# Kernel optimization log

Hardware: AMD Instinct MI355X
Metric: run time of the kernel (lower is better)

## Reference

```python
import jax, jax.numpy as jnp
import numpy as np

V = 50000      # tokenizer vocab size
E = 128        # embedding_dim
H = 160        # encoder_hidden_dim (bidirectional -> 2H)
D = 196        # decoder_hidden_dim
A = 224        # attention_dim
BN = 56        # bottle_neck_dim
PAD, START, END, UNK = 0, 1, 2, 3
COV_FACTOR = 0.75


def _lstm_step(x, h, c, Wi, Wh, bi, bh):
    # torch gate order: i, f, g, o
    g = x @ Wi.T + h @ Wh.T + bi + bh
    i, f, gg, o = jnp.split(g, 4, axis=-1)
    c = jax.nn.sigmoid(f) * c + jax.nn.sigmoid(i) * jnp.tanh(gg)
    h = jax.nn.sigmoid(o) * jnp.tanh(c)
    return h, c


def _run_lstm(x_tbe, Wi, Wh, bi, bh):
    B = x_tbe.shape[1]
    Hh = Wh.shape[1]
    def step(carry, xt):
        h, c = carry
        h, c = _lstm_step(xt, h, c, Wi, Wh, bi, bh)
        return (h, c), h
    init = (jnp.zeros((B, Hh), x_tbe.dtype), jnp.zeros((B, Hh), x_tbe.dtype))
    (hT, cT), hs = jax.lax.scan(step, init, x_tbe)
    return hs, hT, cT


def setup_inputs() -> dict:
    key = jax.random.key(0)
    ks = iter(jax.random.split(key, 48))
    def rn(shape, s=0.05):
        return jax.random.normal(next(ks), shape, jnp.float32) * s
    B, Tin, Ttgt = 32, 256, 100
    inp = {
        'batch_input_ids': jax.random.randint(next(ks), (B, Tin), 0, V + 50, dtype=jnp.int32),
        'batch_target_ids': jax.random.randint(next(ks), (B, Ttgt), 0, V + 50, dtype=jnp.int32),
        'max_num_oovs': 50,
        'emb': rn((V, E), 0.1),
        # bidirectional encoder LSTM
        'Wi_f': rn((4 * H, E)), 'Wh_f': rn((4 * H, H)),
        'bi_f': jnp.zeros(4 * H), 'bh_f': jnp.zeros(4 * H),
        'Wi_b': rn((4 * H, E)), 'Wh_b': rn((4 * H, H)),
        'bi_b': jnp.zeros(4 * H), 'bh_b': jnp.zeros(4 * H),
        # enc->dec bridges
        'Weh': rn((D, 2 * H)), 'beh': jnp.zeros(D),
        'Wec': rn((D, 2 * H)), 'bec': jnp.zeros(D),
        # decoder LSTMCell
        'Wi_d': rn((4 * D, E)), 'Wh_d': rn((4 * D, D)),
        'bi_d': jnp.zeros(4 * D), 'bh_d': jnp.zeros(4 * D),
        # attention
        'Wea': rn((A, 2 * H)), 'bea': jnp.zeros(A),
        'Wda': rn((A, D)),
        'Wca': rn((A, 1)),
        'v_attn': rn((1, A)),
        # vocab projection (bottleneck)
        'W1': rn((BN, D + 2 * H)), 'b1': jnp.zeros(BN),
        'W2': rn((V - END, BN)), 'b2': jnp.zeros(V - END),
        # p_gen switch
        'Wcs': rn((1, 2 * H)), 'bcs': jnp.zeros(1),
        'Wds': rn((1, D)),
        'Wes': rn((1, E)),
    }
    return inp


def reference(batch_input_ids, batch_target_ids, max_num_oovs, emb,
              Wi_f, Wh_f, bi_f, bh_f, Wi_b, Wh_b, bi_b, bh_b,
              Weh, beh, Wec, bec, Wi_d, Wh_d, bi_d, bh_d,
              Wea, bea, Wda, Wca, v_attn, W1, b1, W2, b2,
              Wcs, bcs, Wds, Wes):
    B, Tin = batch_input_ids.shape
    # map OOV input ids to <unk> for embedding lookup
    in_mapped = jnp.where(batch_input_ids >= V, UNK, batch_input_ids)
    x_tbe = emb[in_mapped].transpose(1, 0, 2)          # [Tin,B,E]
    hs_f, hTf, cTf = _run_lstm(x_tbe, Wi_f, Wh_f, bi_f, bh_f)
    hs_b, hTb, cTb = _run_lstm(x_tbe[::-1], Wi_b, Wh_b, bi_b, bh_b)
    enc = jnp.concatenate([hs_f, hs_b[::-1]], -1).transpose(1, 0, 2)  # [B,Tin,2H]
    h = jnp.concatenate([hTf, hTb], -1) @ Weh.T + beh   # [B,D]
    c = jnp.concatenate([cTf, cTb], -1) @ Wec.T + bec   # [B,D]
    enc_attn = enc @ Wea.T + bea                        # [B,Tin,A] (loop-invariant)
    pad_mask = batch_input_ids == PAD
    wca = Wca[:, 0]                                     # [A]
    cov0 = jnp.zeros((B, Tin))
    cur0 = jnp.full((B,), START, jnp.int32)

    def step(carry, nt):
        h, c, cov, cur, nll, cl = carry
        e = emb[cur]                                     # [B,E]
        h, c = _lstm_step(e, h, c, Wi_d, Wh_d, bi_d, bh_d)
        s = jnp.tanh(enc_attn + (h @ Wda.T)[:, None, :] + cov[:, :, None] * wca)
        s = s @ v_attn[0]                                # [B,Tin]
        s = jnp.where(pad_mask, -jnp.inf, s)
        attn = jax.nn.softmax(s, axis=1)                 # [B,Tin]
        ctx = jnp.einsum('bt,bth->bh', attn, enc)        # [B,2H]
        hc = jnp.concatenate([h, ctx], -1)
        vocab = jax.nn.softmax(jnp.tanh(hc @ W1.T + b1) @ W2.T + b2, axis=1)  # [B,V-END]
        p_gen = jax.nn.sigmoid(ctx @ Wcs[0] + bcs[0] + h @ Wds[0] + e @ Wes[0])  # [B]
        # F.pad(vocab, (END, max_num_oovs)).gather(1, nt): left-pad END zeros,
        # right-pad OOV zeros -> gen prob is vocab[nt-END] if END<=nt<V else 0
        idx = jnp.clip(nt - END, 0, vocab.shape[1] - 1)
        gen_p = jnp.take_along_axis(vocab, idx[:, None], axis=1)[:, 0]
        gen_p = jnp.where((nt >= END) & (nt < V), gen_p, 0.0)
        copy_p = jnp.sum(attn * (batch_input_ids == nt[:, None]), axis=1)
        p = p_gen * gen_p + (1.0 - p_gen) * copy_p
        nll = nll - jnp.log(p + 1e-9)
        cl = cl + jnp.minimum(attn, cov).sum(axis=1)
        cov = cov + attn
        cur = jnp.where(nt >= V, UNK, nt)
        return (h, c, cov, cur, nll, cl), None

    (h, c, cov, cur, nll, cl), _ = jax.lax.scan(
        step, (h, c, cov0, cur0, jnp.zeros(B), jnp.zeros(B)), batch_target_ids.T)
    nll_loss = nll.sum()
    cov_loss = cl.sum()
    return nll_loss, cov_loss, nll_loss + COV_FACTOR * cov_loss
```

## Files before the change

kernel.cpp:

```cpp
#include <hip/hip_runtime.h>

#define MSCOPE __HIP_MEMORY_SCOPE_AGENT

typedef __attribute__((ext_vector_type(8))) short bf16x8;
typedef __attribute__((ext_vector_type(4))) float f32x4;


constexpr size_t oXf   = 0;
constexpr size_t oXb   = oXf   + (size_t)8192*640;
constexpr size_t oXd   = oXb   + (size_t)8192*640;
constexpr size_t oHencB= oXd   + (size_t)3200*784;
constexpr size_t oEncA = oHencB+ (size_t)64*256*160;
constexpr size_t oEs   = oEncA + (size_t)8192*224;
constexpr size_t oCT   = oEs   + 3200;
constexpr size_t oH0   = oCT   + 10240;
constexpr size_t oC0   = oH0   + 6272;
constexpr size_t oHWdsAll = oC0 + 6272;
constexpr size_t oCtxWAll = oHWdsAll + 3200;
constexpr size_t oCopyAll = oCtxWAll + 3200;
constexpr size_t oZidxAll = oCopyAll + 3200;
constexpr size_t oClAll   = oZidxAll + 3200;
constexpr size_t oNllWg   = oClAll + 32;
constexpr size_t oW1cT    = oNllWg + 224;
constexpr size_t oAFl     = oW1cT + 17920;
constexpr size_t oAFa     = oAFl + 93184;
constexpr size_t oHdF     = oAFa + 32256;
constexpr size_t oFEnd    = oHdF + 358400;
constexpr size_t oUAll    = 0;
constexpr size_t oUPreAll = oUAll  + (size_t)100*1792;
constexpr size_t oHwdaAll = oUPreAll + (size_t)100*1792;
constexpr size_t oPartAll = oHwdaAll + (size_t)100*7168;
#define FENC(d,t,p)  ((((d)*256 + (t))*20 + (p))*16)
#define FLSTM(s,p)   (163840 + ((s)*8 + (p))*16)
#define FAUX(s,p)    (176640 + ((s)*8 + (p))*16)
#define FP2(s,m,b)   (189440 + (((s)*4 + (m))*32 + (b))*16)
#define CP3          394240
#define CFIN         394256
constexpr int fEnd = 394272;
constexpr unsigned ENC_FULL  = 0xFFFFFu;

__device__ __forceinline__ float fast_tanh(float x){
  float e = __expf(-2.f*fabsf(x));
  float r = (1.f - e) * __builtin_amdgcn_rcpf(1.f + e);
  return copysignf(r, x);
}
__device__ __forceinline__ float sigm(float x){
  return __builtin_amdgcn_rcpf(1.f + __expf(-x));
}
__device__ __forceinline__ unsigned bfr(float f){
  unsigned u = __float_as_uint(f);
  return (u + 0x7FFFu + ((u>>16)&1u)) >> 16;
}
__device__ __forceinline__ float aload(const float* p){
  return __hip_atomic_load(const_cast<float*>(p), __ATOMIC_RELAXED, MSCOPE);
}
__device__ __forceinline__ float2 aload2(const float* p){
  unsigned long long u = __hip_atomic_load(
      reinterpret_cast<unsigned long long*>(const_cast<float*>(p)),
      __ATOMIC_RELAXED, MSCOPE);
  float2 r; __builtin_memcpy(&r, &u, 8); return r;
}
__device__ __forceinline__ void astore(float* p, float v){
  __hip_atomic_store(p, v, __ATOMIC_RELAXED, MSCOPE);
}
__device__ __forceinline__ void astoreu(unsigned* p, unsigned v){
  __hip_atomic_store(p, v, __ATOMIC_RELAXED, MSCOPE);
}
__device__ __forceinline__ void astore2(float* p, float a, float b){
  float2 t; t.x = a; t.y = b;
  unsigned long long u; __builtin_memcpy(&u, &t, 8);
  __hip_atomic_store(reinterpret_cast<unsigned long long*>(p), u,
                     __ATOMIC_RELAXED, MSCOPE);
}
__device__ __forceinline__ unsigned uload(unsigned* p){
  return __hip_atomic_load(p, __ATOMIC_RELAXED, MSCOPE);
}
__device__ __forceinline__ void set_line(unsigned* line){
  __hip_atomic_store(line, 1u, __ATOMIC_RELAXED, MSCOPE);
}
template<int SLP>
__device__ __forceinline__ void wait_lines(unsigned* base, int n, int tid){
  if (tid < 64){
    for(;;){
      bool miss = (tid < n) && (uload(base + tid*16) == 0u);
      if (__ballot(miss) == 0ULL) break;
      __builtin_amdgcn_s_sleep(SLP);
    }
  }
  __syncthreads();
}
__device__ __forceinline__ void add1(unsigned* word){
  (void)__hip_atomic_fetch_add(word, 1u, __ATOMIC_RELAXED, MSCOPE);
}
__device__ __forceinline__ float block_sum(float v, float* red){
  #pragma unroll
  for (int o=32;o;o>>=1) v += __shfl_down(v,o);
  if ((threadIdx.x&63)==0) red[threadIdx.x>>6] = v;
  __syncthreads();
  v = red[0]+red[1]+red[2]+red[3];
  __syncthreads();
  return v;
}

__global__ void prep_kernel(const int* __restrict__ in_ids, const int* __restrict__ tgt,
                            int* __restrict__ in_mapped, int* __restrict__ cur_ids,
                            unsigned* __restrict__ flags, float* __restrict__ hdF){
  const int g0 = blockIdx.x*256 + threadIdx.x, stride = gridDim.x*256;
  for (int i = g0; i < 8192; i += stride){
    int t = i >> 5, b = i & 31;
    int id = in_ids[b*256 + t];
    in_mapped[i] = (id >= 50000) ? 3 : id;
  }
  for (int i = g0; i < 3200; i += stride){
    int k = i >> 5, b = i & 31;
    int id = (k == 0) ? 1 : tgt[b*100 + (k-1)];
    cur_ids[i] = (id >= 50000) ? 3 : id;
  }
  for (int i = g0; i < fEnd; i += stride) flags[i] = 0u;
  for (int i = g0; i < 358400; i += stride) hdF[i] = 0.f;
}

__global__ void w1c_transpose(const float* __restrict__ W1, float* __restrict__ W1cT){
  int i = blockIdx.x*256 + threadIdx.x;
  if (i < 17920){ int q = i / 56, g = i - q*56; W1cT[q*56+g] = W1[(size_t)g*516 + 196 + q]; }
}

__global__ void pack_af(const float* __restrict__ Whd, float* __restrict__ AFl,
                        const float* __restrict__ Wda, const float* __restrict__ W1,
                        const float* __restrict__ Wds, float* __restrict__ AFa){
  int dw = blockIdx.x*256 + threadIdx.x;
  if (dw < 93184){
    int frag = dw>>2, d = dw&3;
    int T = frag/448, r2 = frag - T*448;
    int k7 = r2>>6, l = r2&63;
    int jb = T>>2, gate = T&3;
    int j = jb*16 + (l&15);
    int k0 = k7*32 + ((l>>4)<<3) + 2*d;
    unsigned lo=0, hi=0;
    if (j < 196){
      if (k0   < 196) lo = bfr(Whd[(size_t)(gate*196+j)*196 + k0]);
      if (k0+1 < 196) hi = bfr(Whd[(size_t)(gate*196+j)*196 + k0+1]);
    }
    ((unsigned*)AFl)[dw] = lo | (hi<<16);
  }
  if (dw < 32256){
    int frag = dw>>2, d = dw&3;
    int T = frag/448, r2 = frag - T*448;
    int k7 = r2>>6, l = r2&63;
    int ar = T*16 + (l&15);
    int k0 = k7*32 + ((l>>4)<<3) + 2*d;
    unsigned lo=0, hi=0;
    #pragma unroll
    for (int h = 0; h < 2; ++h){
      int k = k0 + h;
      float v = 0.f;
      if (k < 196){
        if (ar < 224) v = Wda[(size_t)ar*196 + k];
        else { int g = ar - 224;
          if (g < 56) v = W1[(size_t)g*516 + k];
          else if (g == 56) v = Wds[k];
        }
      }
      if (h == 0) lo = bfr(v); else hi = bfr(v);
    }
    ((unsigned*)AFa)[dw] = lo | (hi<<16);
  }
}

struct RGArgs{ const int* gid; const float* emb; const float* W;
               const float* bias1; const float* bias2; float* out; int N; };
__global__ void __launch_bounds__(256) rowgemm(RGArgs a){
  __shared__ float rl[8*128];
  const int tid = threadIdx.x;
  const int N = a.N;
  const size_t r0 = (size_t)blockIdx.x*8;
  const size_t t = r0 >> 5; const int b0 = (int)(r0 & 31);
  for (int i = tid; i < 8*128; i += 256){
    int r = i >> 7, k = i & 127;
    rl[i] = a.emb[(size_t)a.gid[r0+r]*128 + k];
  }
  __syncthreads();
  for (int g = tid; g < N; g += 256){
    const float* wr = a.W + (size_t)g*128;
    float acc[8];
    #pragma unroll
    for (int r=0;r<8;r++) acc[r]=0.f;
    for (int k=0;k<128;k+=4){
      float4 wv = *(const float4*)(wr+k);
      #pragma unroll
      for (int r=0;r<8;r++){
        float4 xv = *(const float4*)(rl + r*128 + k);
        acc[r] += wv.x*xv.x + wv.y*xv.y + wv.z*xv.z + wv.w*xv.w;
      }
    }
    float bias = a.bias1[g] + a.bias2[g];
    float* op = a.out + ((size_t)t*N + g)*32 + b0;
    *(float4*)(op)   = make_float4(acc[0]+bias,acc[1]+bias,acc[2]+bias,acc[3]+bias);
    *(float4*)(op+4) = make_float4(acc[4]+bias,acc[5]+bias,acc[6]+bias,acc[7]+bias);
  }
}

__global__ void es_kernel(const int* __restrict__ gid, const float* __restrict__ emb,
                          const float* __restrict__ Wes, float* __restrict__ es){
  int r = blockIdx.x, l = threadIdx.x;
  const float* e = emb + (size_t)gid[r]*128;
  float acc = e[l]*Wes[l] + e[l+64]*Wes[l+64];
  #pragma unroll
  for (int o=32;o;o>>=1) acc += __shfl_down(acc,o);
  if (l==0) es[r] = acc;
}

struct EncArgs{ const float* Xf; const float* Xb; const float* Whf; const float* Whb;
                float* hencB; float* cT; unsigned* flg; };
__global__ void __launch_bounds__(256) enc_scan(EncArgs a){
  extern __shared__ float sm[];
  float* Wl = sm;
  float* hl = sm + 5120;
  const int wg = blockIdx.x;
  const int dir = wg/20, jwg = wg%20;
  const int tid = threadIdx.x;
  const int b = tid & 31, jl = tid >> 5;
  const int j = jwg*8 + jl;
  const float* Wh = dir ? a.Whb : a.Whf;
  const float* X  = dir ? a.Xb  : a.Xf;
  float* HB = a.hencB + (size_t)dir*32*256*160;
  unsigned* flg = a.flg;
  for (int i = tid; i < 32*160; i += 256){
    int row = i/160, k = i - row*160;
    int gate = row >> 3, jj = row & 7;
    Wl[i] = Wh[((size_t)(gate*160 + jwg*8 + jj))*160 + k];
  }
  for (int i = tid; i < 32*164; i += 256) hl[i] = 0.f;
  float c = 0.f;
  const float4* w0 = (const float4*)(Wl + (0*8+jl)*160);
  const float4* w1 = (const float4*)(Wl + (1*8+jl)*160);
  const float4* w2 = (const float4*)(Wl + (2*8+jl)*160);
  const float4* w3 = (const float4*)(Wl + (3*8+jl)*160);
  __syncthreads();
  for (int t = 0; t < 256; ++t){
    const int trow = dir ? 255 - t : t;
    const float* xr = X + ((size_t)trow*640 + j)*32 + b;
    float g0 = xr[0], g1 = xr[5120], g2 = xr[10240], g3 = xr[15360];
    if (t > 0){
      wait_lines<2>(flg + FENC(dir, t-1, 0), 20, tid);
      const int tprev = dir ? (256 - t) : (t-1);
      for (int i2 = tid; i2 < 2560; i2 += 256){
        int bb = i2/80, kk = (i2 - bb*80)*2;
        float2 v = aload2(HB + ((size_t)bb*256 + tprev)*160 + kk);
        *(float2*)(hl + bb*164 + kk) = v;
      }
    }
    __syncthreads();
    const float4* hr = (const float4*)(hl + b*164);
    #pragma unroll 4
    for (int q = 0; q < 40; ++q){
      float4 hv = hr[q];
      float4 a0 = w0[q], a1 = w1[q], a2 = w2[q], a3 = w3[q];
      g0 += hv.x*a0.x + hv.y*a0.y + hv.z*a0.z + hv.w*a0.w;
      g1 += hv.x*a1.x + hv.y*a1.y + hv.z*a1.z + hv.w*a1.w;
      g2 += hv.x*a2.x + hv.y*a2.y + hv.z*a2.z + hv.w*a2.w;
      g3 += hv.x*a3.x + hv.y*a3.y + hv.z*a3.z + hv.w*a3.w;
    }
    float ig = sigm(g0), fg = sigm(g1), gc = fast_tanh(g2), og = sigm(g3);
    c = fg*c + ig*gc;
    float h = og * fast_tanh(c);
    astore(&HB[((size_t)b*256 + trow)*160 + j], h);
    __syncthreads();
    if (tid == 0) set_line(flg + FENC(dir, t, jwg));
  }
  a.cT[dir*5120 + b*160 + j] = c;
}

__global__ void mid_kernel(const float* __restrict__ hencB, const float* __restrict__ cT,
                           const float* __restrict__ Weh, const float* __restrict__ beh,
                           const float* __restrict__ Wec, const float* __restrict__ bec,
                           float* __restrict__ h0, float* __restrict__ c0){
  __shared__ float hc[320], cc[320];
  int b = blockIdx.x, tid = threadIdx.x;
  if (tid < 160){
    hc[tid]     = hencB[((size_t)b*256 + 255)*160 + tid];
    hc[160+tid] = hencB[((size_t)(32+b)*256 + 0)*160 + tid];
    cc[tid]     = cT[b*160 + tid];
    cc[160+tid] = cT[5120 + b*160 + tid];
  }
  __syncthreads();
  for (int g = tid; g < 196; g += 256){
    const float* w1 = Weh + (size_t)g*320;
    const float* w2 = Wec + (size_t)g*320;
    float a1 = beh[g], a2 = bec[g];
    for (int k = 0; k < 320; ++k){ a1 += hc[k]*w1[k]; a2 += cc[k]*w2[k]; }
    h0[b*196 + g] = a1;
    c0[b*196 + g] = a2;
  }
}

__global__ void __launch_bounds__(256) encA_gemm(const float* __restrict__ hencB,
                 const float* __restrict__ Wea, const float* __restrict__ bea,
                 float* __restrict__ encA){
  __shared__ float rl[8*320];
  const int tid = threadIdx.x;
  const size_t r0 = (size_t)blockIdx.x*8;
  for (int i = tid; i < 8*320; i += 256){
    int r = i/320, k = i - r*320;
    size_t row = r0 + r; int b = (int)(row >> 8), t = (int)(row & 255);
    rl[i] = (k < 160) ? hencB[((size_t)b*256 + t)*160 + k]
                      : hencB[((size_t)(32+b)*256 + t)*160 + (k-160)];
  }
  __syncthreads();
  for (int g = tid; g < 224; g += 256){
    const float* wr = Wea + (size_t)g*320;
    float acc[8];
    #pragma unroll
    for (int r=0;r<8;r++) acc[r]=0.f;
    for (int k=0;k<320;k+=4){
      float4 wv = *(const float4*)(wr+k);
      #pragma unroll
      for (int r=0;r<8;r++){
        float4 xv = *(const float4*)(rl + r*320 + k);
        acc[r] += wv.x*xv.x + wv.y*xv.y + wv.z*xv.z + wv.w*xv.w;
      }
    }
    float bias = bea[g];
    #pragma unroll
    for (int r=0;r<8;r++) encA[(r0+r)*224 + g] = acc[r] + bias;
  }
}

struct DecArgs{
  const float* Xd; const float* hencB; const float* encA;
  const float* h0; const float* c0; const float* AFl; const float* AFa;
  float* hdF;
  const float* Wca; const float* vat; const float* W1cT; const float* b1;
  const float* W2; const float* b2;
  const float* Wcs; const float* bcs; const float* es;
  const int* in_ids; const int* tgt;
  float* uAll; float* uPreAll; float* hwdaAll;
  float* hWdsAll; float* ctxWAll; float* copyAll;
  float* zidxAll; float* partAll; float* clAll; float* nllWg; float* out;
  unsigned* flg;
};

__global__ void __launch_bounds__(256) dec_scan(DecArgs A){
  extern __shared__ float sm[];
  const int wg = blockIdx.x, tid = threadIdx.x;
  unsigned* flg = A.flg;

  if (wg < 8){
    const int q = wg;
    const int nUq  = (q < 5) ? 2 : 1;
    const int jb0q = q;
    const int jb1q = (q < 5) ? q + 8 : 0;
    const int auxB = (q < 5) ? q : (q == 5 ? 5 : (q == 6 ? 9 : 13));
    const int auxC = (q < 5) ? 1 : (q == 7 ? 5 : 4);
    unsigned* ldsu = (unsigned*)sm;
    bf16x8*   ldsf = (bf16x8*)sm;
    const int AB = nUq*1792;
    const int l = tid & 63, wv = tid >> 6;
    const int lq = l >> 4, lc = l & 15;
    const int u = wv >> 1, nt = wv & 1;
    const bool act = u < nUq;
    const int jb = (u == 0) ? jb0q : jb1q;
    {
      const unsigned* aflu = (const unsigned*)A.AFl;
      const unsigned* afau = (const unsigned*)A.AFa;
      const int totDw = (AB + auxC*448)*4;
      for (int i = tid; i < totDw; i += 256){
        int slot = i>>2, d = i&3;
        unsigned v;
        if (slot < AB){
          int uu = slot/1792, r = slot - uu*1792;
          int fi = r>>6, ll = r&63;
          int jbu = (uu == 0) ? jb0q : jb1q;
          int T = jbu*4 + fi/7, k7 = fi%7;
          v = aflu[(((size_t)T*7 + k7)*64 + ll)*4 + d];
        } else {
          int r = slot - AB;
          int a = r/448, r2 = r - a*448;
          int k7 = r2>>6, ll = r2&63;
          v = afau[((((size_t)(auxB + a))*7 + k7)*64 + ll)*4 + d];
        }
        ldsu[i] = v;
      }
    }
    float cst[4];
    if (act){
      int b = nt*16 + lc;
      #pragma unroll
      for (int i = 0; i < 4; ++i){
        int j = jb*16 + lq*4 + i;
        cst[i] = (j < 196) ? A.c0[b*196 + j] : 0.f;
      }
    }
    bf16x8 Bfr[7][2];
    #pragma unroll
    for (int k7 = 0; k7 < 7; ++k7)
      #pragma unroll
      for (int ntt = 0; ntt < 2; ++ntt){
        short tmp[8];
        #pragma unroll
        for (int e = 0; e < 8; ++e){
          int k = k7*32 + lq*8 + e;
          int b = ntt*16 + lc;
          float hv = (k < 196) ? A.h0[b*196 + k] : 0.f;
          tmp[e] = (short)bfr(hv);
        }
        __builtin_memcpy(&Bfr[k7][ntt], tmp, 16);
      }
    __syncthreads();
    unsigned* hdF = (unsigned*)A.hdF;
    for (int s = 0; s < 100; ++s){
      const float* Xs = A.Xd + (size_t)s*25088;
      if (act){
        float xg4[4][4];
        #pragma unroll
        for (int g = 0; g < 4; ++g)
          #pragma unroll
          for (int i = 0; i < 4; ++i){
            int j = jb*16 + lq*4 + i;
            int b = nt*16 + lc;
            xg4[g][i] = (j < 196) ? Xs[((size_t)(g*196 + j))*32 + b] : 0.f;
          }
        f32x4 acc[4];
        #pragma unroll
        for (int g = 0; g < 4; ++g){
          f32x4 a0 = {0.f,0.f,0.f,0.f};
          #pragma unroll
          for (int k7 = 0; k7 < 7; ++k7){
            bf16x8 af = ldsf[(u*28 + g*7 + k7)*64 + l];
            a0 = __builtin_amdgcn_mfma_f32_16x16x32_bf16(af, Bfr[k7][nt], a0, 0,0,0);
          }
          acc[g] = a0;
        }
        float hv4[4];
        #pragma unroll
        for (int i = 0; i < 4; ++i){
          float I = acc[0][i]+xg4[0][i], F = acc[1][i]+xg4[1][i];
          float G = acc[2][i]+xg4[2][i], O = acc[3][i]+xg4[3][i];
          float cc = sigm(F)*cst[i] + sigm(I)*fast_tanh(G);
          cst[i] = cc;
          hv4[i] = sigm(O)*fast_tanh(cc);
        }
        #pragma unroll
        for (int p = 0; p < 2; ++p){
          int jp = jb*16 + lq*4 + 2*p;
          if (jp < 196){
            int k7 = jp>>5, tl = lc | (((jp>>3)&3)<<4), d = (jp&7)>>1;
            unsigned w = bfr(hv4[2*p]) | (bfr(hv4[2*p+1])<<16);
            astoreu(&hdF[(size_t)s*3584 + ((k7*2+nt)*64 + tl)*4 + d], w);
          }
        }
      }
      __syncthreads();
      if (tid == 0) set_line(flg + FLSTM(s, q));
      wait_lines<1>(flg + FLSTM(s, 0), 8, tid);
      {
        const float* hp = (const float*)(hdF + (size_t)s*3584);
        #pragma unroll
        for (int k7 = 0; k7 < 7; ++k7)
          #pragma unroll
          for (int ntt = 0; ntt < 2; ++ntt){
            float2 v0 = aload2(hp + (((k7*2+ntt)*64 + l)*4));
            float2 v1 = aload2(hp + (((k7*2+ntt)*64 + l)*4 + 2));
            unsigned dwv[4];
            __builtin_memcpy(dwv, &v0, 8); __builtin_memcpy(dwv+2, &v1, 8);
            __builtin_memcpy(&Bfr[k7][ntt], dwv, 16);
          }
      }
      for (int a = wv; a < auxC; a += 4){
        int T = auxB + a;
        #pragma unroll
        for (int ntt = 0; ntt < 2; ++ntt){
          f32x4 acc = {0.f,0.f,0.f,0.f};
          #pragma unroll
          for (int k7 = 0; k7 < 7; ++k7){
            bf16x8 af = ldsf[AB + (a*7 + k7)*64 + l];
            acc = __builtin_amdgcn_mfma_f32_16x16x32_bf16(af, Bfr[k7][ntt], acc, 0,0,0);
          }
          int b = ntt*16 + lc;
          #pragma unroll
          for (int p = 0; p < 2; ++p){
            int ar = T*16 + lq*4 + 2*p;
            float v0 = acc[2*p], v1 = acc[2*p+1];
            if (ar < 224){
              astore2(&A.hwdaAll[(size_t)s*7168 + b*224 + ar], v0, v1);
            } else {
              int g = ar - 224;
              if (g < 56) astore2(&A.uPreAll[(size_t)s*1792 + b*56 + g], v0, v1);
              else if (g == 56) astore(&A.hWdsAll[s*32 + b], v0);
            }
          }
        }
      }
      __syncthreads();
      if (tid == 0) set_line(flg + FAUX(s, q));
    }
    return;
  }

  if (wg < 40){
    const int b = wg - 8;
    float* hwdaL = sm;
    float* attnL = sm + 224;
    float* pctx  = sm + 480;
    float* ctxL  = sm + 1440;
    float* red   = sm + 1760;
    float* pu    = sm + 1764;
    float* wcaL  = sm + 1988;
    float* vL    = sm + 2212;
    float* WcsL  = sm + 2436;
    float* b1L   = sm + 2756;
    if (tid < 224){ wcaL[tid] = A.Wca[tid]; vL[tid] = A.vat[tid]; }
    for (int i = tid; i < 320; i += 256) WcsL[i] = A.Wcs[i];
    if (tid < 56) b1L[tid] = A.b1[tid];
    const int inid = A.in_ids[b*256 + tid];
    const float4* erow = (const float4*)(A.encA + (size_t)(b*256 + tid)*224);
    float cov = 0.f, clr = 0.f;
    __syncthreads();
    for (int s = 0; s < 100; ++s){
      wait_lines<2>(flg + FAUX(s, 0), 8, tid);
      if (tid < 224) hwdaL[tid] = aload(&A.hwdaAll[(size_t)s*7168 + b*224 + tid]);
      __syncthreads();
      float exv = 0.f;
      if (inid != 0){
        float acc = 0.f;
        #pragma unroll 8
        for (int q = 0; q < 56; ++q){
          float4 ev = erow[q]; int a0 = 4*q;
          acc += fast_tanh(ev.x + hwdaL[a0]   + cov*wcaL[a0]  )*vL[a0];
          acc += fast_tanh(ev.y + hwdaL[a0+1] + cov*wcaL[a0+1])*vL[a0+1];
          acc += fast_tanh(ev.z + hwdaL[a0+2] + cov*wcaL[a0+2])*vL[a0+2];
          acc += fast_tanh(ev.w + hwdaL[a0+3] + cov*wcaL[a0+3])*vL[a0+3];
        }
        exv = __expf(acc);
      }
      float S = block_sum(exv, red);
      float attn = exv * __builtin_amdgcn_rcpf(S);
      attnL[tid] = attn;
      const int ntb = A.tgt[b*100 + s];
      float cpS = block_sum((inid == ntb) ? attn : 0.f, red);
      float mnS = block_sum(fminf(attn, cov), red);
      if (tid == 0){
        astore(&A.copyAll[s*32 + b], cpS);
        clr += mnS;
        if (s == 99) astore(&A.clAll[b], clr);
      }
      cov += attn;
      if (tid < 240){
        int seg = tid/80, h4i = tid - seg*80;
        int t0 = seg*86, t1 = (t0+86 < 256) ? t0+86 : 256;
        const float* base = (h4i < 40)
          ? (A.hencB + ((size_t)b*256)*160 + (size_t)h4i*4)
          : (A.hencB + ((size_t)(32+b)*256)*160 + (size_t)(h4i-40)*4);
        float4 accv = {0.f,0.f,0.f,0.f};
        #pragma unroll 4
        for (int t2 = t0; t2 < t1; ++t2){
          float av = attnL[t2];
          float4 ev = *(const float4*)(base + (size_t)t2*160);
          accv.x += av*ev.x; accv.y += av*ev.y; accv.z += av*ev.z; accv.w += av*ev.w;
        }
        *(float4*)(pctx + (seg*80+h4i)*4) = accv;
      }
      __syncthreads();
      if (tid < 80){
        float4 p0 = *(float4*)(pctx + tid*4);
        float4 p1 = *(float4*)(pctx + (80+tid)*4);
        float4 p2v = *(float4*)(pctx + (160+tid)*4);
        float4 cvv;
        cvv.x = p0.x+p1.x+p2v.x; cvv.y = p0.y+p1.y+p2v.y;
        cvv.z = p0.z+p1.z+p2v.z; cvv.w = p0.w+p1.w+p2v.w;
        *(float4*)(ctxL + tid*4) = cvv;
      }
      __syncthreads();
      if (tid < 224){
        int g = tid % 56, seg = tid / 56;
        float acc = 0.f;
        const float* wp = A.W1cT + (size_t)seg*80*56 + g;
        #pragma unroll 4
        for (int q = 0; q < 80; ++q) acc += ctxL[seg*80 + q] * wp[q*56];
        pu[seg*56 + g] = acc;
      } else {
        int l = tid - 224; float acc = 0.f;
        for (int q = l; q < 320; q += 32) acc += ctxL[q]*WcsL[q];
        #pragma unroll
        for (int o=16;o;o>>=1) acc += __shfl_down(acc,o,32);
        if (l==0) astore(&A.ctxWAll[s*32 + b], acc);
      }
      __syncthreads();
      if (tid < 56){
        float upre = aload(&A.uPreAll[(size_t)s*1792 + b*56 + tid]);
        float uu = fast_tanh(upre + b1L[tid] + pu[tid] + pu[56+tid] + pu[112+tid] + pu[168+tid]);
        astore(&A.uAll[(size_t)s*1792 + b*56 + tid], uu);
      }
      __syncthreads();
      if (tid == 0){
        set_line(flg + FP2(s,0,b));
        set_line(flg + FP2(s,1,b));
        set_line(flg + FP2(s,2,b));
        set_line(flg + FP2(s,3,b));
      }
    }
    return;
  }

  {
    const int wgv = wg - 40;
    const int vs = (int)(((long long)wgv*49998)/216);
    const int ve = (int)(((long long)(wgv+1)*49998)/216);
    const int v = vs + tid;
    const bool valid = v < ve;
    const int vc = valid ? v : 0;
    float4 w2r[14];
    {
      const float4* wr = (const float4*)(A.W2 + (size_t)vc*56);
      #pragma unroll
      for (int q=0;q<14;++q) w2r[q] = wr[q];
    }
    const float b2v = A.b2[vc];
    float* ulL  = sm;
    float* redW = sm + 1792;
    int*   idxL = (int*)(sm + 1920);
    float* red  = sm + 1952;
    const int lane = tid & 63, wv2 = tid >> 6;
    for (int s = 0; s < 100; ++s){
      int nt3 = (tid < 32) ? A.tgt[tid*100 + s] : 0;
      wait_lines<8>(flg + FP2(s, wgv & 3, 0), 32, tid);
      for (int i2 = tid; i2 < 896; i2 += 256){
        float2 u2 = aload2(&A.uAll[(size_t)s*1792 + i2*2]);
        *(float2*)(ulL + i2*2) = u2;
      }
      if (tid < 32){
        int ix = nt3 - 2; ix = ix<0?0:(ix>49997?49997:ix);
        idxL[tid] = ix;
      }
      __syncthreads();
      #pragma unroll 4
      for (int bb=0; bb<32; ++bb){
        const float4* uv = (const float4*)(ulL + bb*56);
        float z = b2v;
        #pragma unroll
        for (int q=0;q<14;++q){
          float4 u4 = uv[q];
          z += w2r[q].x*u4.x + w2r[q].y*u4.y + w2r[q].z*u4.z + w2r[q].w*u4.w;
        }
        if (valid && v == idxL[bb]) astore(&A.zidxAll[s*32+bb], z);
        float sv2 = valid ? __expf(z) : 0.f;
        #pragma unroll
        for (int o=32;o;o>>=1) sv2 += __shfl_down(sv2,o);
        if (lane == 0) redW[wv2*32+bb] = sv2;
      }
      __syncthreads();
      if (tid < 32){
        float tot = redW[tid]+redW[32+tid]+redW[64+tid]+redW[96+tid];
        astore(&A.partAll[(size_t)(s*32+tid)*216 + wgv], tot);
      }
      __syncthreads();
    }
    __syncthreads();
    if (tid == 0) add1(flg + CP3);
    if (tid == 0){
      while (uload(flg + CP3) != 216u) __builtin_amdgcn_s_sleep(32);
    }
    __syncthreads();
    float nll1 = 0.f;
    for (int p = wgv; p < 3200; p += 216){
      float pv = (tid < 216) ? aload(&A.partAll[(size_t)p*216 + tid]) : 0.f;
      float se = block_sum(pv, red);
      if (tid == 0){
        int s = p >> 5, b = p & 31;
        int nt2 = A.tgt[b*100 + s];
        float xg = aload(&A.ctxWAll[p]) + A.bcs[0] + aload(&A.hWdsAll[p]) + A.es[p];
        float pg = 1.f/(1.f + __expf(-xg));
        float genp = (nt2 >= 2 && nt2 < 50000) ? (__expf(aload(&A.zidxAll[p])) / se) : 0.f;
        float pr = pg*genp + (1.f-pg)*aload(&A.copyAll[p]);
        nll1 += -logf(pr + 1e-9f);
      }
    }
    if (tid == 0) astore(&A.nllWg[wgv], nll1);
    __syncthreads();
    if (tid == 0) add1(flg + CFIN);
    if (wg == 40){
      if (tid == 0){
        while (uload(flg + CFIN) != 216u) __builtin_amdgcn_s_sleep(32);
      }
      __syncthreads();
      float nv = (tid < 216) ? aload(&A.nllWg[tid]) : 0.f;
      float nll = block_sum(nv, red);
      float cv = (tid < 32) ? aload(&A.clAll[tid]) : 0.f;
      float cl = block_sum(cv, red);
      if (tid == 0){ A.out[0]=nll; A.out[1]=cl; A.out[2]=nll + 0.75f*cl; }
    }
  }
}

extern "C" void kernel_launch(void* const* d_in, const int* in_sizes, int n_in,
                              void* d_out, int out_size, void* d_ws, size_t ws_size,
                              hipStream_t stream){
  const int*   in_ids = (const int*)  d_in[0];
  const int*   tgt    = (const int*)  d_in[1];
  const float* emb    = (const float*)d_in[3];
  const float* Wi_f   = (const float*)d_in[4];
  const float* Wh_f   = (const float*)d_in[5];
  const float* bi_f   = (const float*)d_in[6];
  const float* bh_f   = (const float*)d_in[7];
  const float* Wi_b   = (const float*)d_in[8];
  const float* Wh_b   = (const float*)d_in[9];
  const float* bi_b   = (const float*)d_in[10];
  const float* bh_b   = (const float*)d_in[11];
  const float* Weh    = (const float*)d_in[12];
  const float* beh    = (const float*)d_in[13];
  const float* Wec    = (const float*)d_in[14];
  const float* bec    = (const float*)d_in[15];
  const float* Wi_d   = (const float*)d_in[16];
  const float* Wh_d   = (const float*)d_in[17];
  const float* bi_d   = (const float*)d_in[18];
  const float* bh_d   = (const float*)d_in[19];
  const float* Wea    = (const float*)d_in[20];
  const float* bea    = (const float*)d_in[21];
  const float* Wda    = (const float*)d_in[22];
  const float* Wca    = (const float*)d_in[23];
  const float* vat    = (const float*)d_in[24];
  const float* W1     = (const float*)d_in[25];
  const float* b1     = (const float*)d_in[26];
  const float* W2     = (const float*)d_in[27];
  const float* b2     = (const float*)d_in[28];
  const float* Wcs    = (const float*)d_in[29];
  const float* bcs    = (const float*)d_in[30];
  const float* Wds    = (const float*)d_in[31];
  const float* Wes    = (const float*)d_in[32];

  float* ws = (float*)d_ws;
  int* iBase = (int*)(ws + oFEnd);
  int* in_mapped = iBase;
  int* cur_ids   = iBase + 8192;
  unsigned* flags = (unsigned*)(iBase + 11392);

  prep_kernel<<<512, 256, 0, stream>>>(in_ids, tgt, in_mapped, cur_ids, flags,
                                       ws + oHdF);
  w1c_transpose<<<70, 256, 0, stream>>>(W1, ws + oW1cT);
  pack_af<<<364, 256, 0, stream>>>(Wh_d, ws + oAFl, Wda, W1, Wds, ws + oAFa);

  { RGArgs a{in_mapped, emb, Wi_f, bi_f, bh_f, ws + oXf, 640};
    rowgemm<<<1024, 256, 0, stream>>>(a); }
  { RGArgs a{in_mapped, emb, Wi_b, bi_b, bh_b, ws + oXb, 640};
    rowgemm<<<1024, 256, 0, stream>>>(a); }
  { RGArgs a{cur_ids, emb, Wi_d, bi_d, bh_d, ws + oXd, 784};
    rowgemm<<<400, 256, 0, stream>>>(a); }

  es_kernel<<<3200, 64, 0, stream>>>(cur_ids, emb, Wes, ws + oEs);

  { EncArgs ea{ws + oXf, ws + oXb, Wh_f, Wh_b, ws + oHencB, ws + oCT, flags};
    void* ka[] = {&ea};
    hipLaunchCooperativeKernel((void*)enc_scan, dim3(40), dim3(256), ka,
                               (unsigned)((5120 + 32*164)*4), stream); }

  mid_kernel<<<32, 256, 0, stream>>>(ws + oHencB, ws + oCT, Weh, beh, Wec, bec,
                                     ws + oH0, ws + oC0);

  encA_gemm<<<1024, 256, 0, stream>>>(ws + oHencB, Wea, bea, ws + oEncA);

  { DecArgs da{ws + oXd, ws + oHencB, ws + oEncA,
               ws + oH0, ws + oC0, ws + oAFl, ws + oAFa,
               ws + oHdF,
               Wca, vat, ws + oW1cT, b1, W2, b2, Wcs, bcs, ws + oEs,
               in_ids, tgt,
               ws + oUAll, ws + oUPreAll, ws + oHwdaAll,
               ws + oHWdsAll, ws + oCtxWAll, ws + oCopyAll,
               ws + oZidxAll, ws + oPartAll, ws + oClAll, ws + oNllWg, (float*)d_out,
               flags};
    dec_scan<<<dim3(256), dim3(256), 64512, stream>>>(da); }
}
```

Baseline: 4.650 ms.

## Fold independent prep work into encoder scan launch and move encA GEMM into decoder

The decoder-input GEMM, weight packing, W1 transpose and es dot products now run as extra blocks of the same launch as the 40-block encoder recurrence, so they fill otherwise idle CUs while the latency-bound scan runs. The separate encA GEMM kernel is removed. Its work is now done inside the decoder's vocab workgroups before their main loop, and a counter flag tells the attention workgroups when encA is complete. This removes several launches and hides their work behind the serial scan. In exchange, the encoder scan is no longer a cooperative launch, so it relies on its 40 spin-waiting blocks all being resident at once. The encA GEMM also becomes a less efficient one-row-at-a-time loop on the decoder's critical path.

```diff
diff --git a/kernel.cpp b/kernel.cpp
--- a/kernel.cpp
+++ b/kernel.cpp
@@ -36,7 +36,8 @@
 #define FP2(s,m,b)   (189440 + (((s)*4 + (m))*32 + (b))*16)
 #define CP3          394240
 #define CFIN         394256
-constexpr int fEnd = 394272;
+#define CENC         394272
+constexpr int fEnd = 394288;
 constexpr unsigned ENC_FULL  = 0xFFFFFu;
 
 __device__ __forceinline__ float fast_tanh(float x){
@@ -118,53 +119,6 @@
   }
   for (int i = g0; i < fEnd; i += stride) flags[i] = 0u;
   for (int i = g0; i < 358400; i += stride) hdF[i] = 0.f;
-}
-
-__global__ void w1c_transpose(const float* __restrict__ W1, float* __restrict__ W1cT){
-  int i = blockIdx.x*256 + threadIdx.x;
-  if (i < 17920){ int q = i / 56, g = i - q*56; W1cT[q*56+g] = W1[(size_t)g*516 + 196 + q]; }
-}
-
-__global__ void pack_af(const float* __restrict__ Whd, float* __restrict__ AFl,
-                        const float* __restrict__ Wda, const float* __restrict__ W1,
-                        const float* __restrict__ Wds, float* __restrict__ AFa){
-  int dw = blockIdx.x*256 + threadIdx.x;
-  if (dw < 93184){
-    int frag = dw>>2, d = dw&3;
-    int T = frag/448, r2 = frag - T*448;
-    int k7 = r2>>6, l = r2&63;
-    int jb = T>>2, gate = T&3;
-    int j = jb*16 + (l&15);
-    int k0 = k7*32 + ((l>>4)<<3) + 2*d;
-    unsigned lo=0, hi=0;
-    if (j < 196){
-      if (k0   < 196) lo = bfr(Whd[(size_t)(gate*196+j)*196 + k0]);
-      if (k0+1 < 196) hi = bfr(Whd[(size_t)(gate*196+j)*196 + k0+1]);
-    }
-    ((unsigned*)AFl)[dw] = lo | (hi<<16);
-  }
-  if (dw < 32256){
-    int frag = dw>>2, d = dw&3;
-    int T = frag/448, r2 = frag - T*448;
-    int k7 = r2>>6, l = r2&63;
-    int ar = T*16 + (l&15);
-    int k0 = k7*32 + ((l>>4)<<3) + 2*d;
-    unsigned lo=0, hi=0;
-    #pragma unroll
-    for (int h = 0; h < 2; ++h){
-      int k = k0 + h;
-      float v = 0.f;
-      if (k < 196){
-        if (ar < 224) v = Wda[(size_t)ar*196 + k];
-        else { int g = ar - 224;
-          if (g < 56) v = W1[(size_t)g*516 + k];
-          else if (g == 56) v = Wds[k];
-        }
-      }
-      if (h == 0) lo = bfr(v); else hi = bfr(v);
-    }
-    ((unsigned*)AFa)[dw] = lo | (hi<<16);
-  }
 }
 
 struct RGArgs{ const int* gid; const float* emb; const float* W;
@@ -200,75 +154,166 @@
   }
 }
 
-__global__ void es_kernel(const int* __restrict__ gid, const float* __restrict__ emb,
-                          const float* __restrict__ Wes, float* __restrict__ es){
-  int r = blockIdx.x, l = threadIdx.x;
-  const float* e = emb + (size_t)gid[r]*128;
-  float acc = e[l]*Wes[l] + e[l+64]*Wes[l+64];
-  #pragma unroll
-  for (int o=32;o;o>>=1) acc += __shfl_down(acc,o);
-  if (l==0) es[r] = acc;
-}
-
-struct EncArgs{ const float* Xf; const float* Xb; const float* Whf; const float* Whb;
-                float* hencB; float* cT; unsigned* flg; };
-__global__ void __launch_bounds__(256) enc_scan(EncArgs a){
+struct MegaArgs{
+  const float* Xf; const float* Xb; const float* Whf; const float* Whb;
+  float* hencB; float* cT; unsigned* flg;
+  const int* cur_ids; const float* emb;
+  const float* Wi_d; const float* bi_d; const float* bh_d; float* Xd;
+  const float* Whd; float* AFl;
+  const float* Wda; const float* W1; const float* Wds; float* AFa;
+  float* W1cT;
+  const float* Wes; float* es;
+};
+
+__global__ void __launch_bounds__(256) enc_mega(MegaArgs a){
   extern __shared__ float sm[];
-  float* Wl = sm;
-  float* hl = sm + 5120;
-  const int wg = blockIdx.x;
-  const int dir = wg/20, jwg = wg%20;
-  const int tid = threadIdx.x;
-  const int b = tid & 31, jl = tid >> 5;
-  const int j = jwg*8 + jl;
-  const float* Wh = dir ? a.Whb : a.Whf;
-  const float* X  = dir ? a.Xb  : a.Xf;
-  float* HB = a.hencB + (size_t)dir*32*256*160;
-  unsigned* flg = a.flg;
-  for (int i = tid; i < 32*160; i += 256){
-    int row = i/160, k = i - row*160;
-    int gate = row >> 3, jj = row & 7;
-    Wl[i] = Wh[((size_t)(gate*160 + jwg*8 + jj))*160 + k];
-  }
-  for (int i = tid; i < 32*164; i += 256) hl[i] = 0.f;
-  float c = 0.f;
-  const float4* w0 = (const float4*)(Wl + (0*8+jl)*160);
-  const float4* w1 = (const float4*)(Wl + (1*8+jl)*160);
-  const float4* w2 = (const float4*)(Wl + (2*8+jl)*160);
-  const float4* w3 = (const float4*)(Wl + (3*8+jl)*160);
-  __syncthreads();
-  for (int t = 0; t < 256; ++t){
-    const int trow = dir ? 255 - t : t;
-    const float* xr = X + ((size_t)trow*640 + j)*32 + b;
-    float g0 = xr[0], g1 = xr[5120], g2 = xr[10240], g3 = xr[15360];
-    if (t > 0){
-      wait_lines<2>(flg + FENC(dir, t-1, 0), 20, tid);
-      const int tprev = dir ? (256 - t) : (t-1);
-      for (int i2 = tid; i2 < 2560; i2 += 256){
-        int bb = i2/80, kk = (i2 - bb*80)*2;
-        float2 v = aload2(HB + ((size_t)bb*256 + tprev)*160 + kk);
-        *(float2*)(hl + bb*164 + kk) = v;
-      }
-    }
+  const int blk = blockIdx.x, tid = threadIdx.x;
+
+  if (blk < 40){
+    float* Wl = sm;
+    float* hl = sm + 5120;
+    const int dir = blk/20, jwg = blk%20;
+    const int b = tid & 31, jl = tid >> 5;
+    const int j = jwg*8 + jl;
+    const float* Wh = dir ? a.Whb : a.Whf;
+    const float* X  = dir ? a.Xb  : a.Xf;
+    float* HB = a.hencB + (size_t)dir*32*256*160;
+    unsigned* flg = a.flg;
+    for (int i = tid; i < 32*160; i += 256){
+      int row = i/160, k = i - row*160;
+      int gate = row >> 3, jj = row & 7;
+      Wl[i] = Wh[((size_t)(gate*160 + jwg*8 + jj))*160 + k];
+    }
+    for (int i = tid; i < 32*164; i += 256) hl[i] = 0.f;
+    float c = 0.f;
+    const float4* w0 = (const float4*)(Wl + (0*8+jl)*160);
+    const float4* w1 = (const float4*)(Wl + (1*8+jl)*160);
+    const float4* w2 = (const float4*)(Wl + (2*8+jl)*160);
+    const float4* w3 = (const float4*)(Wl + (3*8+jl)*160);
     __syncthreads();
-    const float4* hr = (const float4*)(hl + b*164);
-    #pragma unroll 4
-    for (int q = 0; q < 40; ++q){
-      float4 hv = hr[q];
-      float4 a0 = w0[q], a1 = w1[q], a2 = w2[q], a3 = w3[q];
-      g0 += hv.x*a0.x + hv.y*a0.y + hv.z*a0.z + hv.w*a0.w;
-      g1 += hv.x*a1.x + hv.y*a1.y + hv.z*a1.z + hv.w*a1.w;
-      g2 += hv.x*a2.x + hv.y*a2.y + hv.z*a2.z + hv.w*a2.w;
-      g3 += hv.x*a3.x + hv.y*a3.y + hv.z*a3.z + hv.w*a3.w;
-    }
-    float ig = sigm(g0), fg = sigm(g1), gc = fast_tanh(g2), og = sigm(g3);
-    c = fg*c + ig*gc;
-    float h = og * fast_tanh(c);
-    astore(&HB[((size_t)b*256 + trow)*160 + j], h);
+    for (int t = 0; t < 256; ++t){
+      const int trow = dir ? 255 - t : t;
+      const float* xr = X + ((size_t)trow*640 + j)*32 + b;
+      float g0 = xr[0], g1 = xr[5120], g2 = xr[10240], g3 = xr[15360];
+      if (t > 0){
+        wait_lines<2>(flg + FENC(dir, t-1, 0), 20, tid);
+        const int tprev = dir ? (256 - t) : (t-1);
+        for (int i2 = tid; i2 < 2560; i2 += 256){
+          int bb = i2/80, kk = (i2 - bb*80)*2;
+          float2 v = aload2(HB + ((size_t)bb*256 + tprev)*160 + kk);
+          *(float2*)(hl + bb*164 + kk) = v;
+        }
+      }
+      __syncthreads();
+      const float4* hr = (const float4*)(hl + b*164);
+      #pragma unroll 4
+      for (int q = 0; q < 40; ++q){
+        float4 hv = hr[q];
+        float4 a0 = w0[q], a1 = w1[q], a2 = w2[q], a3 = w3[q];
+        g0 += hv.x*a0.x + hv.y*a0.y + hv.z*a0.z + hv.w*a0.w;
+        g1 += hv.x*a1.x + hv.y*a1.y + hv.z*a1.z + hv.w*a1.w;
+        g2 += hv.x*a2.x + hv.y*a2.y + hv.z*a2.z + hv.w*a2.w;
+        g3 += hv.x*a3.x + hv.y*a3.y + hv.z*a3.z + hv.w*a3.w;
+      }
+      float ig = sigm(g0), fg = sigm(g1), gc = fast_tanh(g2), og = sigm(g3);
+      c = fg*c + ig*gc;
+      float h = og * fast_tanh(c);
+      astore(&HB[((size_t)b*256 + trow)*160 + j], h);
+      __syncthreads();
+      if (tid == 0) set_line(flg + FENC(dir, t, jwg));
+    }
+    a.cT[dir*5120 + b*160 + j] = c;
+    return;
+  }
+
+  if (blk < 440){
+    float* rl = sm;
+    const size_t r0 = (size_t)(blk - 40)*8;
+    const size_t t = r0 >> 5; const int b0 = (int)(r0 & 31);
+    for (int i = tid; i < 8*128; i += 256){
+      int r = i >> 7, k = i & 127;
+      rl[i] = a.emb[(size_t)a.cur_ids[r0+r]*128 + k];
+    }
     __syncthreads();
-    if (tid == 0) set_line(flg + FENC(dir, t, jwg));
-  }
-  a.cT[dir*5120 + b*160 + j] = c;
+    for (int g = tid; g < 784; g += 256){
+      const float* wr = a.Wi_d + (size_t)g*128;
+      float acc[8];
+      #pragma unroll
+      for (int r=0;r<8;r++) acc[r]=0.f;
+      for (int k=0;k<128;k+=4){
+        float4 wv = *(const float4*)(wr+k);
+        #pragma unroll
+        for (int r=0;r<8;r++){
+          float4 xv = *(const float4*)(rl + r*128 + k);
+          acc[r] += wv.x*xv.x + wv.y*xv.y + wv.z*xv.z + wv.w*xv.w;
+        }
+      }
+      float bias = a.bi_d[g] + a.bh_d[g];
+      float* op = a.Xd + ((size_t)t*784 + g)*32 + b0;
+      *(float4*)(op)   = make_float4(acc[0]+bias,acc[1]+bias,acc[2]+bias,acc[3]+bias);
+      *(float4*)(op+4) = make_float4(acc[4]+bias,acc[5]+bias,acc[6]+bias,acc[7]+bias);
+    }
+    return;
+  }
+
+  if (blk < 804){
+    int dw = (blk - 440)*256 + tid;
+    if (dw < 93184){
+      int frag = dw>>2, d = dw&3;
+      int T = frag/448, r2 = frag - T*448;
+      int k7 = r2>>6, l = r2&63;
+      int jb = T>>2, gate = T&3;
+      int j = jb*16 + (l&15);
+      int k0 = k7*32 + ((l>>4)<<3) + 2*d;
+      unsigned lo=0, hi=0;
+      if (j < 196){
+        if (k0   < 196) lo = bfr(a.Whd[(size_t)(gate*196+j)*196 + k0]);
+        if (k0+1 < 196) hi = bfr(a.Whd[(size_t)(gate*196+j)*196 + k0+1]);
+      }
+      ((unsigned*)a.AFl)[dw] = lo | (hi<<16);
+    }
+    if (dw < 32256){
+      int frag = dw>>2, d = dw&3;
+      int T = frag/448, r2 = frag - T*448;
+      int k7 = r2>>6, l = r2&63;
+      int ar = T*16 + (l&15);
+      int k0 = k7*32 + ((l>>4)<<3) + 2*d;
+      unsigned lo=0, hi=0;
+      #pragma unroll
+      for (int h = 0; h < 2; ++h){
+        int k = k0 + h;
+        float v = 0.f;
+        if (k < 196){
+          if (ar < 224) v = a.Wda[(size_t)ar*196 + k];
+          else { int g = ar - 224;
+            if (g < 56) v = a.W1[(size_t)g*516 + k];
+            else if (g == 56) v = a.Wds[k];
+          }
+        }
+        if (h == 0) lo = bfr(v); else hi = bfr(v);
+      }
+      ((unsigned*)a.AFa)[dw] = lo | (hi<<16);
+    }
+    return;
+  }
+
+  if (blk < 874){
+    int i = (blk - 804)*256 + tid;
+    if (i < 17920){ int q = i / 56, g = i - q*56; a.W1cT[q*56+g] = a.W1[(size_t)g*516 + 196 + q]; }
+    return;
+  }
+
+  {
+    int r = (blk - 874)*4 + (tid >> 6);
+    int l = tid & 63;
+    if (r < 3200){
+      const float* e = a.emb + (size_t)a.cur_ids[r]*128;
+      float acc = e[l]*a.Wes[l] + e[l+64]*a.Wes[l+64];
+      #pragma unroll
+      for (int o=32;o;o>>=1) acc += __shfl_down(acc,o);
+      if (l==0) a.es[r] = acc;
+    }
+  }
 }
 
 __global__ void mid_kernel(const float* __restrict__ hencB, const float* __restrict__ cT,
@@ -294,42 +339,11 @@
   }
 }
 
-__global__ void __launch_bounds__(256) encA_gemm(const float* __restrict__ hencB,
-                 const float* __restrict__ Wea, const float* __restrict__ bea,
-                 float* __restrict__ encA){
-  __shared__ float rl[8*320];
-  const int tid = threadIdx.x;
-  const size_t r0 = (size_t)blockIdx.x*8;
-  for (int i = tid; i < 8*320; i += 256){
-    int r = i/320, k = i - r*320;
-    size_t row = r0 + r; int b = (int)(row >> 8), t = (int)(row & 255);
-    rl[i] = (k < 160) ? hencB[((size_t)b*256 + t)*160 + k]
-                      : hencB[((size_t)(32+b)*256 + t)*160 + (k-160)];
-  }
-  __syncthreads();
-  for (int g = tid; g < 224; g += 256){
-    const float* wr = Wea + (size_t)g*320;
-    float acc[8];
-    #pragma unroll
-    for (int r=0;r<8;r++) acc[r]=0.f;
-    for (int k=0;k<320;k+=4){
-      float4 wv = *(const float4*)(wr+k);
-      #pragma unroll
-      for (int r=0;r<8;r++){
-        float4 xv = *(const float4*)(rl + r*320 + k);
-        acc[r] += wv.x*xv.x + wv.y*xv.y + wv.z*xv.z + wv.w*xv.w;
-      }
-    }
-    float bias = bea[g];
-    #pragma unroll
-    for (int r=0;r<8;r++) encA[(r0+r)*224 + g] = acc[r] + bias;
-  }
-}
-
 struct DecArgs{
-  const float* Xd; const float* hencB; const float* encA;
+  const float* Xd; const float* hencB; float* encA;
   const float* h0; const float* c0; const float* AFl; const float* AFa;
   float* hdF;
+  const float* Wea; const float* bea;
   const float* Wca; const float* vat; const float* W1cT; const float* b1;
   const float* W2; const float* b2;
   const float* Wcs; const float* bcs; const float* es;
@@ -515,6 +529,9 @@
     const int inid = A.in_ids[b*256 + tid];
     const float4* erow = (const float4*)(A.encA + (size_t)(b*256 + tid)*224);
     float cov = 0.f, clr = 0.f;
+    if (tid == 0){
+      while (uload(flg + CENC) != 216u) __builtin_amdgcn_s_sleep(8);
+    }
     __syncthreads();
     for (int s = 0; s < 100; ++s){
       wait_lines<2>(flg + FAUX(s, 0), 8, tid);
@@ -604,6 +621,32 @@
 
   {
     const int wgv = wg - 40;
+    {
+      float* hlrow = sm;
+      for (int rr = 0; rr < 38; ++rr){
+        int row = wgv*38 + rr;
+        if (row < 8192){
+          int b = row >> 8, t = row & 255;
+          for (int k = tid; k < 320; k += 256)
+            hlrow[k] = (k < 160) ? A.hencB[((size_t)b*256 + t)*160 + k]
+                                 : A.hencB[((size_t)(32+b)*256 + t)*160 + (k-160)];
+          __syncthreads();
+          if (tid < 224){
+            const float* wr = A.Wea + (size_t)tid*320;
+            float acc = A.bea[tid];
+            for (int k = 0; k < 320; k += 4){
+              float4 wv = *(const float4*)(wr+k);
+              float4 xv = *(const float4*)(hlrow+k);
+              acc += wv.x*xv.x + wv.y*xv.y + wv.z*xv.z + wv.w*xv.w;
+            }
+            astore(&A.encA[(size_t)row*224 + tid], acc);
+          }
+          __syncthreads();
+        }
+      }
+      __syncthreads();
+      if (tid == 0) add1(flg + CENC);
+    }
     const int vs = (int)(((long long)wgv*49998)/216);
     const int ve = (int)(((long long)(wgv+1)*49998)/216);
     const int v = vs + tid;
@@ -736,31 +779,25 @@
 
   prep_kernel<<<512, 256, 0, stream>>>(in_ids, tgt, in_mapped, cur_ids, flags,
                                        ws + oHdF);
-  w1c_transpose<<<70, 256, 0, stream>>>(W1, ws + oW1cT);
-  pack_af<<<364, 256, 0, stream>>>(Wh_d, ws + oAFl, Wda, W1, Wds, ws + oAFa);
 
   { RGArgs a{in_mapped, emb, Wi_f, bi_f, bh_f, ws + oXf, 640};
     rowgemm<<<1024, 256, 0, stream>>>(a); }
   { RGArgs a{in_mapped, emb, Wi_b, bi_b, bh_b, ws + oXb, 640};
     rowgemm<<<1024, 256, 0, stream>>>(a); }
-  { RGArgs a{cur_ids, emb, Wi_d, bi_d, bh_d, ws + oXd, 784};
-    rowgemm<<<400, 256, 0, stream>>>(a); }
-
-  es_kernel<<<3200, 64, 0, stream>>>(cur_ids, emb, Wes, ws + oEs);
-
-  { EncArgs ea{ws + oXf, ws + oXb, Wh_f, Wh_b, ws + oHencB, ws + oCT, flags};
-    void* ka[] = {&ea};
-    hipLaunchCooperativeKernel((void*)enc_scan, dim3(40), dim3(256), ka,
-                               (unsigned)((5120 + 32*164)*4), stream); }
+
+  { MegaArgs ma{ws + oXf, ws + oXb, Wh_f, Wh_b, ws + oHencB, ws + oCT, flags,
+                cur_ids, emb, Wi_d, bi_d, bh_d, ws + oXd,
+                Wh_d, ws + oAFl, Wda, W1, Wds, ws + oAFa,
+                ws + oW1cT, Wes, ws + oEs};
+    enc_mega<<<dim3(1674), dim3(256), (5120 + 32*164)*4, stream>>>(ma); }
 
   mid_kernel<<<32, 256, 0, stream>>>(ws + oHencB, ws + oCT, Weh, beh, Wec, bec,
                                      ws + oH0, ws + oC0);
-
-  encA_gemm<<<1024, 256, 0, stream>>>(ws + oHencB, Wea, bea, ws + oEncA);
 
   { DecArgs da{ws + oXd, ws + oHencB, ws + oEncA,
                ws + oH0, ws + oC0, ws + oAFl, ws + oAFa,
                ws + oHdF,
+               Wea, bea,
                Wca, vat, ws + oW1cT, b1, W2, b2, Wcs, bcs, ws + oEs,
                in_ids, tgt,
                ws + oUAll, ws + oUPreAll, ws + oHwdaAll,
```

Measured after the change: 4.866 ms. +4.6%, slower.
